# Kernel optimization log

Hardware: AMD Instinct MI355X
Metric: run time of the kernel (lower is better)

The kernel has to match this reference:

```python
import jax, jax.numpy as jnp
import numpy as np

B, C, H, W = 8, 1, 384, 384
P, D, NH, L, E, HF = 16, 768, 12, 12, 4, 3072
Hp, Wp = H // P, W // P
N = Hp * Wp            # 576 tokens
DH = D // NH           # 64 per head
EPS = 1e-5


def setup_inputs() -> dict:
    key = jax.random.key(0)
    ks = jax.random.split(key, 10)
    g = lambda k, shp: (0.02 * jax.random.normal(k, shp, dtype=jnp.float32))
    return {
        "x": jax.random.normal(ks[0], (B, C, H, W), dtype=jnp.float32),
        "patch_w": g(ks[1], (D, C * P * P)),        # Conv2d(k=16,s=16) == unfold+matmul
        "patch_b": jnp.zeros((D,), jnp.float32),
        "pos_embed": g(ks[2], (1, N, D)),
        "ln1_g": jnp.ones((L, D), jnp.float32),
        "ln1_b": jnp.zeros((L, D), jnp.float32),
        "qkv_w": g(ks[3], (L, 3 * D, D)),           # torch MHA in_proj_weight
        "qkv_b": jnp.zeros((L, 3 * D), jnp.float32),
        "out_w": g(ks[4], (L, D, D)),
        "out_b": jnp.zeros((L, D), jnp.float32),
        "ln2_g": jnp.ones((L, D), jnp.float32),
        "ln2_b": jnp.zeros((L, D), jnp.float32),
        "gate_w": g(ks[5], (L, E, D)),
        "gate_b": jnp.zeros((L, E), jnp.float32),
        "w1": g(ks[6], (L, E, HF, D)),
        "b1": jnp.zeros((L, E, HF), jnp.float32),
        "w2": g(ks[7], (L, E, D, HF)),
        "b2": jnp.zeros((L, E, D), jnp.float32),
    }


def _ln(x, g, b):
    m = jnp.mean(x, -1, keepdims=True)
    v = jnp.var(x, -1, keepdims=True)
    return (x - m) * jax.lax.rsqrt(v + EPS) * g + b


def _layer(t, prm):
    (l1g, l1b, qw, qb, ow, ob, l2g, l2b, gw, gb, W1, B1, W2, B2) = prm
    # --- MHA (pre-LN, residual) ---
    h = _ln(t, l1g, l1b)
    qkv = h @ qw.T + qb                                   # [B,N,3D]
    q, k, v = jnp.split(qkv, 3, axis=-1)
    q = q.reshape(B, N, NH, DH).transpose(0, 2, 1, 3)     # [B,NH,N,DH]
    k = k.reshape(B, N, NH, DH).transpose(0, 2, 1, 3)
    v = v.reshape(B, N, NH, DH).transpose(0, 2, 1, 3)
    att = jax.nn.softmax(jnp.einsum('bhnd,bhmd->bhnm', q, k) / jnp.sqrt(jnp.float32(DH)), axis=-1)
    a = jnp.einsum('bhnm,bhmd->bhnd', att, v).transpose(0, 2, 1, 3).reshape(B, N, D)
    t = t + a @ ow.T + ob
    # --- MoE FFN, top_k=1: raw gate logits used as combine weights ---
    h2 = _ln(t, l2g, l2b)
    scores = h2 @ gw.T + gb                               # [B,N,E]
    idx = jnp.argmax(scores, axis=-1)                     # [B,N] chosen expert
    wgt = jnp.max(scores, axis=-1)                        # [B,N] raw logit weight
    hid = jax.nn.gelu(jnp.einsum('bnd,ehd->benh', h2, W1) + B1[None, :, None, :], approximate=False)
    y = jnp.einsum('benh,edh->bend', hid, W2) + B2[None, :, None, :]   # [B,E,N,D]
    sel = jax.nn.one_hot(idx, E, dtype=t.dtype) * wgt[..., None]       # [B,N,E]
    t = t + jnp.einsum('bend,bne->bnd', y, sel)
    return t, None


def reference(x, patch_w, patch_b, pos_embed, ln1_g, ln1_b, qkv_w, qkv_b,
              out_w, out_b, ln2_g, ln2_b, gate_w, gate_b, w1, b1, w2, b2):
    # patch embed: Conv2d(kernel=stride=P) == non-overlapping unfold + matmul
    patches = x.reshape(B, C, Hp, P, Wp, P).transpose(0, 2, 4, 1, 3, 5).reshape(B, N, C * P * P)
    tok = patches @ patch_w.T + patch_b + pos_embed
    layer = jax.checkpoint(_layer)
    tok, _ = jax.lax.scan(layer, tok,
                          (ln1_g, ln1_b, qkv_w, qkv_b, out_w, out_b,
                           ln2_g, ln2_b, gate_w, gate_b, w1, b1, w2, b2))
    # rearrange 'b (h w) c -> b c h w'
    return tok.reshape(B, Hp, Wp, D).transpose(0, 3, 1, 2)
```

## Files before the change

kernel.cpp:

```cpp
#include <hip/hip_runtime.h>
#include <cmath>

#define TOK 4608
#define DMODEL 768

typedef __attribute__((ext_vector_type(8))) _Float16 f16x8;
typedef __attribute__((ext_vector_type(4))) float f32x4;

__device__ __forceinline__ float gelu_exact(float x) {
    return 0.5f * x * (1.0f + erff(x * 0.70710678118654752440f));
}

__device__ __forceinline__ void cvt2(float x, unsigned short& h, unsigned short& m)
{
    _Float16 hf = (_Float16)x;
    float r = (x - (float)hf) * 2048.0f;
    _Float16 mf = (_Float16)r;
    h = __builtin_bit_cast(unsigned short, hf);
    m = __builtin_bit_cast(unsigned short, mf);
}

__device__ __forceinline__ void cvt2_pack8(const float4 a, const float4 b,
                                           uint4& H, uint4& M)
{
    unsigned short h[8], m[8];
    cvt2(a.x, h[0], m[0]); cvt2(a.y, h[1], m[1]);
    cvt2(a.z, h[2], m[2]); cvt2(a.w, h[3], m[3]);
    cvt2(b.x, h[4], m[4]); cvt2(b.y, h[5], m[5]);
    cvt2(b.z, h[6], m[6]); cvt2(b.w, h[7], m[7]);
    H = (uint4){ (unsigned)h[0] | ((unsigned)h[1] << 16), (unsigned)h[2] | ((unsigned)h[3] << 16),
                 (unsigned)h[4] | ((unsigned)h[5] << 16), (unsigned)h[6] | ((unsigned)h[7] << 16) };
    M = (uint4){ (unsigned)m[0] | ((unsigned)m[1] << 16), (unsigned)m[2] | ((unsigned)m[3] << 16),
                 (unsigned)m[4] | ((unsigned)m[5] << 16), (unsigned)m[6] | ((unsigned)m[7] << 16) };
}

__global__ __launch_bounds__(256)
void im2col_kernel(const float* __restrict__ x, float* __restrict__ patches)
{
    int idx = blockIdx.x*256 + threadIdx.x;
    int k = idx & 255, tokid = idx >> 8;
    int b = tokid / 576, n = tokid % 576;
    int hp = n / 24, wp = n % 24;
    patches[idx] = x[(size_t)b*147456 + (size_t)(hp*16 + (k >> 4))*384 + wp*16 + (k & 15)];
}

__global__ __launch_bounds__(256)
void ln_kernel(const float* __restrict__ in, float* __restrict__ out,
               const float* __restrict__ g, const float* __restrict__ bta)
{
    int tokid = blockIdx.x;
    const float* xr = in + (size_t)tokid*768;
    int t = threadIdx.x;
    float v0 = xr[t], v1 = xr[t+256], v2 = xr[t+512];
    float s = v0+v1+v2, q = v0*v0+v1*v1+v2*v2;
    for (int off = 32; off > 0; off >>= 1) {
        s += __shfl_down(s, off);
        q += __shfl_down(q, off);
    }
    __shared__ float ss[4], sq[4];
    int wv = t >> 6, ln = t & 63;
    if (ln == 0) { ss[wv] = s; sq[wv] = q; }
    __syncthreads();
    float ts = ss[0]+ss[1]+ss[2]+ss[3];
    float tq = sq[0]+sq[1]+sq[2]+sq[3];
    float mean = ts * (1.f/768.f);
    float var  = tq * (1.f/768.f) - mean*mean;
    float inv  = rsqrtf(var + 1e-5f);
    float* orow = out + (size_t)tokid*768;
    orow[t]     = (v0-mean)*inv*g[t]     + bta[t];
    orow[t+256] = (v1-mean)*inv*g[t+256] + bta[t+256];
    orow[t+512] = (v2-mean)*inv*g[t+512] + bta[t+512];
}

template<bool SWZ>
__global__ __launch_bounds__(256, 2)
void gemm_big(const float* __restrict__ A, const float* __restrict__ Bw,
              const float* __restrict__ bias, float* __restrict__ C,
              int M, int Nout, int K, int ldA, int ldC, int mode,
              const int* __restrict__ lists, const int* __restrict__ counts,
              const float* __restrict__ wgt)
{
    int Meff = M;
    const int* gather = nullptr;
    if (counts) {
        int e = blockIdx.z;
        Meff   = counts[e];
        gather = lists + e * TOK;
        Bw    += (size_t)e * Nout * K;
        bias  += (size_t)e * Nout;
    }
    int m0, n0;
    if constexpr (SWZ) {
        int gx  = gridDim.x;
        int nwg = gx * gridDim.y;
        int bid = blockIdx.y * gx + blockIdx.x;
        bid = (bid & 7) * (nwg >> 3) + (bid >> 3);
        m0 = (bid / gx) << 7; n0 = (bid % gx) << 7;
    } else {
        m0 = blockIdx.y << 7; n0 = blockIdx.x << 7;
    }
    if (m0 >= Meff) return;

    __shared__ unsigned short Ah[128][40];
    __shared__ unsigned short Am[128][40];
    __shared__ unsigned short Bh[128][40];
    __shared__ unsigned short Bm[128][40];

    int t = threadIdx.x;
    int srow = t >> 1;
    int koff = (t & 1) << 4;

    int ar = m0 + srow;
    long agrow = -1;
    if (ar < Meff) agrow = gather ? gather[ar] : ar;
    const float* Asrc = (agrow >= 0) ? (A + (size_t)agrow*ldA + koff) : nullptr;
    const float* Bsrc = Bw + (size_t)(n0 + srow)*K + koff;

    int lane = t & 63;
    int wv   = t >> 6;
    int wm   = (wv >> 1) << 6;
    int wn   = (wv & 1) << 6;
    int r16  = lane & 15;
    int g    = lane >> 4;

    f32x4 acc1[4][4], acc2[4][4];
    #pragma unroll
    for (int i = 0; i < 4; ++i)
        #pragma unroll
        for (int j = 0; j < 4; ++j) {
            acc1[i][j] = (f32x4){0.f, 0.f, 0.f, 0.f};
            acc2[i][j] = (f32x4){0.f, 0.f, 0.f, 0.f};
        }

    float4 ra[4], rb[4];
    ra[0] = ra[1] = ra[2] = ra[3] = make_float4(0.f, 0.f, 0.f, 0.f);

    auto load_tile = [&](int k0) {
        if (Asrc) {
            ra[0] = *(const float4*)(Asrc + k0);
            ra[1] = *(const float4*)(Asrc + k0 + 4);
            ra[2] = *(const float4*)(Asrc + k0 + 8);
            ra[3] = *(const float4*)(Asrc + k0 + 12);
        }
        rb[0] = *(const float4*)(Bsrc + k0);
        rb[1] = *(const float4*)(Bsrc + k0 + 4);
        rb[2] = *(const float4*)(Bsrc + k0 + 8);
        rb[3] = *(const float4*)(Bsrc + k0 + 12);
    };

    load_tile(0);

    for (int k0 = 0; k0 < K; k0 += 32) {
        __syncthreads();
        {
            uint4 H, M_;
            cvt2_pack8(ra[0], ra[1], H, M_);
            *(uint4*)&Ah[srow][koff]   = H;
            *(uint4*)&Am[srow][koff]   = M_;
            cvt2_pack8(ra[2], ra[3], H, M_);
            *(uint4*)&Ah[srow][koff+8] = H;
            *(uint4*)&Am[srow][koff+8] = M_;
            cvt2_pack8(rb[0], rb[1], H, M_);
            *(uint4*)&Bh[srow][koff]   = H;
            *(uint4*)&Bm[srow][koff]   = M_;
            cvt2_pack8(rb[2], rb[3], H, M_);
            *(uint4*)&Bh[srow][koff+8] = H;
            *(uint4*)&Bm[srow][koff+8] = M_;
        }
        __syncthreads();
        if (k0 + 32 < K) load_tile(k0 + 32);

        f16x8 fah[4], fam[4];
        #pragma unroll
        for (int i = 0; i < 4; ++i) {
            int ml = wm + i*16 + r16;
            fah[i] = *(const f16x8*)&Ah[ml][g*8];
            fam[i] = *(const f16x8*)&Am[ml][g*8];
        }
        #pragma unroll
        for (int j = 0; j < 4; ++j) {
            int nl = wn + j*16 + r16;
            f16x8 fbh = *(const f16x8*)&Bh[nl][g*8];
            f16x8 fbm = *(const f16x8*)&Bm[nl][g*8];
            #pragma unroll
            for (int i = 0; i < 4; ++i) {
                acc1[i][j] = __builtin_amdgcn_mfma_f32_16x16x32_f16(fah[i], fbh, acc1[i][j], 0, 0, 0);
                acc2[i][j] = __builtin_amdgcn_mfma_f32_16x16x32_f16(fah[i], fbm, acc2[i][j], 0, 0, 0);
                acc2[i][j] = __builtin_amdgcn_mfma_f32_16x16x32_f16(fam[i], fbh, acc2[i][j], 0, 0, 0);
            }
        }
    }

    const float MS = 1.0f / 2048.0f;
    float biasv[4];
    #pragma unroll
    for (int j = 0; j < 4; ++j) biasv[j] = bias[n0 + wn + j*16 + r16];

    #pragma unroll
    for (int i = 0; i < 4; ++i) {
        int mb = m0 + wm + i*16 + (g << 2);
        #pragma unroll
        for (int r = 0; r < 4; ++r) {
            int m = mb + r;
            if (m >= Meff) continue;
            int row = gather ? gather[m] : m;
            size_t rowoff = (size_t)row*ldC + n0 + wn + r16;
            float w = (mode == 3) ? wgt[row] : 0.f;
            #pragma unroll
            for (int j = 0; j < 4; ++j) {
                float val = acc1[i][j][r] + acc2[i][j][r] * MS + biasv[j];
                size_t off = rowoff + j*16;
                if      (mode == 0) C[off] = val;
                else if (mode == 1) C[off] += val;
                else if (mode == 2) C[off] = gelu_exact(val);
                else if (mode == 3) C[off] += w * val;
                else C[off] = val + wgt[(size_t)(row % 576)*768 + n0 + wn + j*16 + r16];
            }
        }
    }
}

template<bool SWZ>
__global__ __launch_bounds__(256, 2)
void gemm_small(const float* __restrict__ A, const float* __restrict__ Bw,
                const float* __restrict__ bias, float* __restrict__ C,
                int M, int Nout, int K, int ldA, int ldC, int mode,
                const int* __restrict__ lists, const int* __restrict__ counts,
                const float* __restrict__ wgt)
{
    int Meff = M;
    const int* gather = nullptr;
    if (counts) {
        int e = blockIdx.z;
        Meff   = counts[e];
        gather = lists + e * TOK;
        Bw    += (size_t)e * Nout * K;
        bias  += (size_t)e * Nout;
    }
    int m0, n0;
    if constexpr (SWZ) {
        int gx  = gridDim.x;
        int nwg = gx * gridDim.y;
        int bid = blockIdx.y * gx + blockIdx.x;
        bid = (bid & 7) * (nwg >> 3) + (bid >> 3);
        m0 = (bid / gx) << 6; n0 = (bid % gx) << 6;
    } else {
        m0 = blockIdx.y << 6; n0 = blockIdx.x << 6;
    }
    if (m0 >= Meff) return;

    __shared__ unsigned short Ah[64][72];
    __shared__ unsigned short Am[64][72];
    __shared__ unsigned short Bh[64][72];
    __shared__ unsigned short Bm[64][72];

    int t = threadIdx.x;
    int srow  = t >> 1;
    int khalf = (t & 1) << 5;
    bool isA = srow < 64;
    int row  = isA ? srow : (srow - 64);

    const float* src = nullptr;
    if (isA) {
        int ar = m0 + row;
        if (ar < Meff) {
            long agrow = gather ? gather[ar] : ar;
            src = A + (size_t)agrow*ldA + khalf;
        }
    } else {
        src = Bw + (size_t)(n0 + row)*K + khalf;
    }

    int lane = t & 63;
    int wv   = t >> 6;
    int wm   = (wv >> 1) << 5;
    int wn   = (wv & 1) << 5;
    int r16  = lane & 15;
    int g    = lane >> 4;

    f32x4 acc1[2][2], acc2[2][2];
    #pragma unroll
    for (int i = 0; i < 2; ++i)
        #pragma unroll
        for (int j = 0; j < 2; ++j) {
            acc1[i][j] = (f32x4){0.f, 0.f, 0.f, 0.f};
            acc2[i][j] = (f32x4){0.f, 0.f, 0.f, 0.f};
        }

    float4 rr[8];
    #pragma unroll
    for (int i = 0; i < 8; ++i) rr[i] = make_float4(0.f, 0.f, 0.f, 0.f);

    auto load_tile = [&](int k0) {
        if (src) {
            #pragma unroll
            for (int i = 0; i < 8; ++i) rr[i] = *(const float4*)(src + k0 + 4*i);
        }
    };

    load_tile(0);

    for (int k0 = 0; k0 < K; k0 += 64) {
        __syncthreads();
        {
            unsigned short (*Xh)[72] = isA ? Ah : Bh;
            unsigned short (*Xm)[72] = isA ? Am : Bm;
            #pragma unroll
            for (int i = 0; i < 8; i += 2) {
                uint4 H, M_;
                cvt2_pack8(rr[i], rr[i+1], H, M_);
                *(uint4*)&Xh[row][khalf + 4*i] = H;
                *(uint4*)&Xm[row][khalf + 4*i] = M_;
            }
        }
        __syncthreads();
        if (k0 + 64 < K) load_tile(k0 + 64);

        #pragma unroll
        for (int ks = 0; ks < 2; ++ks) {
            f16x8 fah[2], fam[2];
            #pragma unroll
            for (int i = 0; i < 2; ++i) {
                int ml = wm + i*16 + r16;
                fah[i] = *(const f16x8*)&Ah[ml][ks*32 + g*8];
                fam[i] = *(const f16x8*)&Am[ml][ks*32 + g*8];
            }
            #pragma unroll
            for (int j = 0; j < 2; ++j) {
                int nl = wn + j*16 + r16;
                f16x8 fbh = *(const f16x8*)&Bh[nl][ks*32 + g*8];
                f16x8 fbm = *(const f16x8*)&Bm[nl][ks*32 + g*8];
                #pragma unroll
                for (int i = 0; i < 2; ++i) {
                    acc1[i][j] = __builtin_amdgcn_mfma_f32_16x16x32_f16(fah[i], fbh, acc1[i][j], 0, 0, 0);
                    acc2[i][j] = __builtin_amdgcn_mfma_f32_16x16x32_f16(fah[i], fbm, acc2[i][j], 0, 0, 0);
                    acc2[i][j] = __builtin_amdgcn_mfma_f32_16x16x32_f16(fam[i], fbh, acc2[i][j], 0, 0, 0);
                }
            }
        }
    }

    const float MS = 1.0f / 2048.0f;
    float biasv[2];
    #pragma unroll
    for (int j = 0; j < 2; ++j) biasv[j] = bias[n0 + wn + j*16 + r16];

    #pragma unroll
    for (int i = 0; i < 2; ++i) {
        int mb = m0 + wm + i*16 + (g << 2);
        #pragma unroll
        for (int r = 0; r < 4; ++r) {
            int m = mb + r;
            if (m >= Meff) continue;
            int rowc = gather ? gather[m] : m;
            size_t rowoff = (size_t)rowc*ldC + n0 + wn + r16;
            float w = (mode == 3) ? wgt[rowc] : 0.f;
            #pragma unroll
            for (int j = 0; j < 2; ++j) {
                float val = acc1[i][j][r] + acc2[i][j][r] * MS + biasv[j];
                size_t off = rowoff + j*16;
                if      (mode == 0) C[off] = val;
                else if (mode == 1) C[off] += val;
                else if (mode == 2) C[off] = gelu_exact(val);
                else if (mode == 3) C[off] += w * val;
                else C[off] = val + wgt[(size_t)(rowc % 576)*768 + n0 + wn + j*16 + r16];
            }
        }
    }
}

__global__ __launch_bounds__(256)
void attn_kernel(const float* __restrict__ qkv, float* __restrict__ attn)
{
    int q0 = blockIdx.x << 6;
    int h  = blockIdx.y;
    int b  = blockIdx.z;
    const float* base = qkv + (size_t)b * 576 * 2304;
    int qoff = h << 6, koff = 768 + (h << 6), voff = 1536 + (h << 6);

    __shared__ unsigned short Qh[64][72], Qm[64][72];
    __shared__ unsigned short Kh[64][72], Km[64][72];
    __shared__ unsigned short Vth[64][72], Vtm[64][72];
    __shared__ unsigned short Ph[64][72], Pm[64][72];

    int t    = threadIdx.x;
    int lane = t & 63;
    int wq   = t >> 6;
    int l15  = lane & 15;
    int g    = lane >> 4;

    int srow = t >> 2;
    int sq   = t & 3;

    {
        const float* src = &base[(size_t)(q0 + srow)*2304 + qoff + (sq << 4)];
        #pragma unroll
        for (int k = 0; k < 16; k += 4) {
            float4 v = *(const float4*)(src + k);
            ushort4 hh, mm;
            cvt2(v.x, hh.x, mm.x); cvt2(v.y, hh.y, mm.y);
            cvt2(v.z, hh.z, mm.z); cvt2(v.w, hh.w, mm.w);
            *(ushort4*)&Qh[srow][(sq << 4) + k] = hh;
            *(ushort4*)&Qm[srow][(sq << 4) + k] = mm;
        }
    }
    __syncthreads();

    f16x8 fqh[2], fqm[2];
    #pragma unroll
    for (int ks = 0; ks < 2; ++ks) {
        fqh[ks] = *(const f16x8*)&Qh[wq*16 + l15][ks*32 + g*8];
        fqm[ks] = *(const f16x8*)&Qm[wq*16 + l15][ks*32 + g*8];
    }

    float4 rk[4], rv[4];
    {
        const float* ks_ = &base[(size_t)srow*2304 + koff + (sq << 4)];
        const float* vs_ = &base[(size_t)srow*2304 + voff + (sq << 2)];
        #pragma unroll
        for (int k = 0; k < 4; ++k) rk[k] = *(const float4*)(ks_ + 4*k);
        #pragma unroll
        for (int k = 0; k < 4; ++k) rv[k] = *(const float4*)(vs_ + 16*k);
    }

    f32x4 o1[4], o2[4];
    #pragma unroll
    for (int df = 0; df < 4; ++df) {
        o1[df] = (f32x4){0.f,0.f,0.f,0.f};
        o2[df] = (f32x4){0.f,0.f,0.f,0.f};
    }
    float m_[4] = {-3.4e38f,-3.4e38f,-3.4e38f,-3.4e38f};
    float l_[4] = {0.f,0.f,0.f,0.f};
    const float MS = 1.0f / 2048.0f;

    for (int j0 = 0; j0 < 576; j0 += 64) {
        __syncthreads();
        #pragma unroll
        for (int k = 0; k < 4; ++k) {
            ushort4 hh, mm;
            cvt2(rk[k].x, hh.x, mm.x); cvt2(rk[k].y, hh.y, mm.y);
            cvt2(rk[k].z, hh.z, mm.z); cvt2(rk[k].w, hh.w, mm.w);
            *(ushort4*)&Kh[srow][(sq << 4) + 4*k] = hh;
            *(ushort4*)&Km[srow][(sq << 4) + 4*k] = mm;
        }
        #pragma unroll
        for (int k = 0; k < 4; ++k) {
            ushort4 hh, mm;
            cvt2(rv[k].x, hh.x, mm.x); cvt2(rv[k].y, hh.y, mm.y);
            cvt2(rv[k].z, hh.z, mm.z); cvt2(rv[k].w, hh.w, mm.w);
            int dbase = (sq << 2) + (k << 4);
            Vth[dbase+0][srow] = hh.x; Vtm[dbase+0][srow] = mm.x;
            Vth[dbase+1][srow] = hh.y; Vtm[dbase+1][srow] = mm.y;
            Vth[dbase+2][srow] = hh.z; Vtm[dbase+2][srow] = mm.z;
            Vth[dbase+3][srow] = hh.w; Vtm[dbase+3][srow] = mm.w;
        }
        __syncthreads();
        int jn = j0 + 64;
        if (jn < 576) {
            const float* ks_ = &base[(size_t)(jn + srow)*2304 + koff + (sq << 4)];
            const float* vs_ = &base[(size_t)(jn + srow)*2304 + voff + (sq << 2)];
            #pragma unroll
            for (int k = 0; k < 4; ++k) rk[k] = *(const float4*)(ks_ + 4*k);
            #pragma unroll
            for (int k = 0; k < 4; ++k) rv[k] = *(const float4*)(vs_ + 16*k);
        }

        f32x4 s1[4], s2[4];
        #pragma unroll
        for (int jf = 0; jf < 4; ++jf) {
            s1[jf] = (f32x4){0.f,0.f,0.f,0.f};
            s2[jf] = (f32x4){0.f,0.f,0.f,0.f};
        }
        #pragma unroll
        for (int jf = 0; jf < 4; ++jf) {
            #pragma unroll
            for (int ks = 0; ks < 2; ++ks) {
                f16x8 fkh = *(const f16x8*)&Kh[jf*16 + l15][ks*32 + g*8];
                f16x8 fkm = *(const f16x8*)&Km[jf*16 + l15][ks*32 + g*8];
                s1[jf] = __builtin_amdgcn_mfma_f32_16x16x32_f16(fqh[ks], fkh, s1[jf], 0, 0, 0);
                s2[jf] = __builtin_amdgcn_mfma_f32_16x16x32_f16(fqh[ks], fkm, s2[jf], 0, 0, 0);
                s2[jf] = __builtin_amdgcn_mfma_f32_16x16x32_f16(fqm[ks], fkh, s2[jf], 0, 0, 0);
            }
        }
        float p[4][4];
        #pragma unroll
        for (int jf = 0; jf < 4; ++jf)
            #pragma unroll
            for (int r = 0; r < 4; ++r)
                p[jf][r] = (s1[jf][r] + s2[jf][r]*MS) * 0.125f;

        #pragma unroll
        for (int r = 0; r < 4; ++r) {
            float tm = fmaxf(fmaxf(p[0][r], p[1][r]), fmaxf(p[2][r], p[3][r]));
            #pragma unroll
            for (int off = 8; off > 0; off >>= 1) tm = fmaxf(tm, __shfl_xor(tm, off, 16));
            float mn = fmaxf(m_[r], tm);
            float f  = expf(m_[r] - mn);
            m_[r] = mn;
            l_[r] *= f;
            #pragma unroll
            for (int df = 0; df < 4; ++df) { o1[df][r] *= f; o2[df][r] *= f; }
            float ps = 0.f;
            #pragma unroll
            for (int jf = 0; jf < 4; ++jf) {
                p[jf][r] = expf(p[jf][r] - mn);
                ps += p[jf][r];
            }
            #pragma unroll
            for (int off = 8; off > 0; off >>= 1) ps += __shfl_xor(ps, off, 16);
            l_[r] += ps;
        }
        #pragma unroll
        for (int jf = 0; jf < 4; ++jf)
            #pragma unroll
            for (int r = 0; r < 4; ++r) {
                unsigned short ph, pm;
                cvt2(p[jf][r], ph, pm);
                Ph[wq*16 + g*4 + r][jf*16 + l15] = ph;
                Pm[wq*16 + g*4 + r][jf*16 + l15] = pm;
            }

        #pragma unroll
        for (int ks = 0; ks < 2; ++ks) {
            f16x8 fph = *(const f16x8*)&Ph[wq*16 + l15][ks*32 + g*8];
            f16x8 fpm = *(const f16x8*)&Pm[wq*16 + l15][ks*32 + g*8];
            #pragma unroll
            for (int df = 0; df < 4; ++df) {
                f16x8 fvh = *(const f16x8*)&Vth[df*16 + l15][ks*32 + g*8];
                f16x8 fvm = *(const f16x8*)&Vtm[df*16 + l15][ks*32 + g*8];
                o1[df] = __builtin_amdgcn_mfma_f32_16x16x32_f16(fph, fvh, o1[df], 0, 0, 0);
                o2[df] = __builtin_amdgcn_mfma_f32_16x16x32_f16(fph, fvm, o2[df], 0, 0, 0);
                o2[df] = __builtin_amdgcn_mfma_f32_16x16x32_f16(fpm, fvh, o2[df], 0, 0, 0);
            }
        }
    }

    #pragma unroll
    for (int r = 0; r < 4; ++r) {
        float inv = 1.f / l_[r];
        size_t row = (size_t)(b*576 + q0 + wq*16 + g*4 + r)*768 + qoff + l15;
        #pragma unroll
        for (int df = 0; df < 4; ++df)
            attn[row + df*16] = (o1[df][r] + o2[df][r]*MS) * inv;
    }
}

__global__ __launch_bounds__(256)
void gate_kernel(const float* __restrict__ h2, const float* __restrict__ gw,
                 const float* __restrict__ gb, float* __restrict__ wgt,
                 int* __restrict__ lists, int* __restrict__ counts)
{
    int tokid = blockIdx.x;
    int t = threadIdx.x;
    const float* hr = h2 + (size_t)tokid*768;
    float p0=0.f,p1=0.f,p2=0.f,p3=0.f;
    for (int k = t; k < 768; k += 256) {
        float hv = hr[k];
        p0 = fmaf(hv, gw[k],        p0);
        p1 = fmaf(hv, gw[768 + k],  p1);
        p2 = fmaf(hv, gw[1536 + k], p2);
        p3 = fmaf(hv, gw[2304 + k], p3);
    }
    for (int off = 32; off > 0; off >>= 1) {
        p0 += __shfl_down(p0, off);
        p1 += __shfl_down(p1, off);
        p2 += __shfl_down(p2, off);
        p3 += __shfl_down(p3, off);
    }
    __shared__ float red[4][4];
    int wv = t >> 6, ln = t & 63;
    if (ln == 0) { red[wv][0]=p0; red[wv][1]=p1; red[wv][2]=p2; red[wv][3]=p3; }
    __syncthreads();
    if (t == 0) {
        float s[4];
        #pragma unroll
        for (int e = 0; e < 4; ++e)
            s[e] = red[0][e]+red[1][e]+red[2][e]+red[3][e] + gb[e];
        int best = 0; float bv = s[0];
        #pragma unroll
        for (int e = 1; e < 4; ++e) if (s[e] > bv) { bv = s[e]; best = e; }
        wgt[tokid] = bv;
        int pos = atomicAdd(&counts[best], 1);
        lists[best*TOK + pos] = tokid;
    }
}

__global__ void zero_counts(int* counts) { if (threadIdx.x < 4) counts[threadIdx.x] = 0; }

__global__ __launch_bounds__(256)
void out_transpose(const float* __restrict__ tok, float* __restrict__ out)
{
    int idx = blockIdx.x*256 + threadIdx.x;
    int wp = idx % 24;
    int hp = (idx / 24) % 24;
    int d  = (idx / 576) % 768;
    int b  = idx / (576*768);
    out[idx] = tok[(size_t)(b*576 + hp*24 + wp)*768 + d];
}

extern "C" void kernel_launch(void* const* d_in, const int* in_sizes, int n_in,
                              void* d_out, int out_size, void* d_ws, size_t ws_size,
                              hipStream_t stream)
{
    const float* x       = (const float*)d_in[0];
    const float* patch_w = (const float*)d_in[1];
    const float* patch_b = (const float*)d_in[2];
    const float* pos     = (const float*)d_in[3];
    const float* ln1_g   = (const float*)d_in[4];
    const float* ln1_b   = (const float*)d_in[5];
    const float* qkv_w   = (const float*)d_in[6];
    const float* qkv_b   = (const float*)d_in[7];
    const float* out_w   = (const float*)d_in[8];
    const float* out_b   = (const float*)d_in[9];
    const float* ln2_g   = (const float*)d_in[10];
    const float* ln2_b   = (const float*)d_in[11];
    const float* gate_w  = (const float*)d_in[12];
    const float* gate_b  = (const float*)d_in[13];
    const float* w1      = (const float*)d_in[14];
    const float* b1      = (const float*)d_in[15];
    const float* w2      = (const float*)d_in[16];
    const float* b2      = (const float*)d_in[17];
    float* out = (float*)d_out;

    float* ws    = (float*)d_ws;
    float* tok   = ws;
    float* h     = ws + 3538944;
    float* scr   = ws + 7077888;
    float* qkv   = scr;
    float* attn  = scr + 10616832;
    float* hid   = scr;
    float* patches = scr;
    float* wgt   = ws + 21233664;
    int*   lists = (int*)(ws + 21238272);
    int*   counts= (int*)(ws + 21256704);

    im2col_kernel<<<4608, 256, 0, stream>>>(x, patches);
    gemm_small<true><<<dim3(12,72,1), 256, 0, stream>>>(patches, patch_w, patch_b, tok,
                                                        4608, 768, 256, 256, 768, 4,
                                                        nullptr, nullptr, pos);

    for (int l = 0; l < 12; ++l) {
        ln_kernel<<<4608, 256, 0, stream>>>(tok, h, ln1_g + l*768, ln1_b + l*768);
        gemm_big<true><<<dim3(18,36,1), 256, 0, stream>>>(h, qkv_w + (size_t)l*1769472,
                                                          qkv_b + l*2304, qkv,
                                                          4608, 2304, 768, 768, 2304, 0,
                                                          nullptr, nullptr, nullptr);
        attn_kernel<<<dim3(9,12,8), 256, 0, stream>>>(qkv, attn);
        gemm_small<true><<<dim3(12,72,1), 256, 0, stream>>>(attn, out_w + (size_t)l*589824,
                                                            out_b + l*768, tok,
                                                            4608, 768, 768, 768, 768, 1,
                                                            nullptr, nullptr, nullptr);
        ln_kernel<<<4608, 256, 0, stream>>>(tok, h, ln2_g + l*768, ln2_b + l*768);
        zero_counts<<<1, 64, 0, stream>>>(counts);
        gate_kernel<<<4608, 256, 0, stream>>>(h, gate_w + l*3072, gate_b + l*4, wgt, lists, counts);
        gemm_big<false><<<dim3(24,36,4), 256, 0, stream>>>(h, w1 + (size_t)l*9437184,
                                                           b1 + (size_t)l*4*3072, hid,
                                                           4608, 3072, 768, 768, 3072, 2,
                                                           lists, counts, nullptr);
        gemm_small<false><<<dim3(12,72,4), 256, 0, stream>>>(hid, w2 + (size_t)l*9437184,
                                                             b2 + (size_t)l*4*768, tok,
                                                             4608, 768, 3072, 3072, 768, 3,
                                                             lists, counts, wgt);
    }
    out_transpose<<<13824, 256, 0, stream>>>(tok, out);
}
```

Baseline: 8.257 ms.

## Double-buffer shared-memory tiles in split-fp16 GEMM kernels to drop one barrier

Both GEMM kernels now keep two shared-memory buffers per operand. The next tile is converted and stored into the alternate buffer after the MFMA work on the current one, so only one __syncthreads is needed per k-step instead of two. The aim is to cut barrier stalls and overlap staging with compute. In exchange, shared-memory use per block doubles, which may reduce occupancy.

```diff
diff --git a/kernel.cpp b/kernel.cpp
--- a/kernel.cpp
+++ b/kernel.cpp
@@ -101,10 +101,10 @@
     }
     if (m0 >= Meff) return;
 
-    __shared__ unsigned short Ah[128][40];
-    __shared__ unsigned short Am[128][40];
-    __shared__ unsigned short Bh[128][40];
-    __shared__ unsigned short Bm[128][40];
+    __shared__ unsigned short Ah[2][128][40];
+    __shared__ unsigned short Am[2][128][40];
+    __shared__ unsigned short Bh[2][128][40];
+    __shared__ unsigned short Bm[2][128][40];
 
     int t = threadIdx.x;
     int srow = t >> 1;
@@ -148,40 +148,43 @@
         rb[3] = *(const float4*)(Bsrc + k0 + 12);
     };
 
+    auto stage = [&](int buf) {
+        uint4 H, M_;
+        cvt2_pack8(ra[0], ra[1], H, M_);
+        *(uint4*)&Ah[buf][srow][koff]   = H;
+        *(uint4*)&Am[buf][srow][koff]   = M_;
+        cvt2_pack8(ra[2], ra[3], H, M_);
+        *(uint4*)&Ah[buf][srow][koff+8] = H;
+        *(uint4*)&Am[buf][srow][koff+8] = M_;
+        cvt2_pack8(rb[0], rb[1], H, M_);
+        *(uint4*)&Bh[buf][srow][koff]   = H;
+        *(uint4*)&Bm[buf][srow][koff]   = M_;
+        cvt2_pack8(rb[2], rb[3], H, M_);
+        *(uint4*)&Bh[buf][srow][koff+8] = H;
+        *(uint4*)&Bm[buf][srow][koff+8] = M_;
+    };
+
     load_tile(0);
+    stage(0);
+    int cur = 0;
 
     for (int k0 = 0; k0 < K; k0 += 32) {
         __syncthreads();
-        {
-            uint4 H, M_;
-            cvt2_pack8(ra[0], ra[1], H, M_);
-            *(uint4*)&Ah[srow][koff]   = H;
-            *(uint4*)&Am[srow][koff]   = M_;
-            cvt2_pack8(ra[2], ra[3], H, M_);
-            *(uint4*)&Ah[srow][koff+8] = H;
-            *(uint4*)&Am[srow][koff+8] = M_;
-            cvt2_pack8(rb[0], rb[1], H, M_);
-            *(uint4*)&Bh[srow][koff]   = H;
-            *(uint4*)&Bm[srow][koff]   = M_;
-            cvt2_pack8(rb[2], rb[3], H, M_);
-            *(uint4*)&Bh[srow][koff+8] = H;
-            *(uint4*)&Bm[srow][koff+8] = M_;
-        }
-        __syncthreads();
-        if (k0 + 32 < K) load_tile(k0 + 32);
+        bool more = (k0 + 32 < K);
+        if (more) load_tile(k0 + 32);
 
         f16x8 fah[4], fam[4];
         #pragma unroll
         for (int i = 0; i < 4; ++i) {
             int ml = wm + i*16 + r16;
-            fah[i] = *(const f16x8*)&Ah[ml][g*8];
-            fam[i] = *(const f16x8*)&Am[ml][g*8];
+            fah[i] = *(const f16x8*)&Ah[cur][ml][g*8];
+            fam[i] = *(const f16x8*)&Am[cur][ml][g*8];
         }
         #pragma unroll
         for (int j = 0; j < 4; ++j) {
             int nl = wn + j*16 + r16;
-            f16x8 fbh = *(const f16x8*)&Bh[nl][g*8];
-            f16x8 fbm = *(const f16x8*)&Bm[nl][g*8];
+            f16x8 fbh = *(const f16x8*)&Bh[cur][nl][g*8];
+            f16x8 fbm = *(const f16x8*)&Bm[cur][nl][g*8];
             #pragma unroll
             for (int i = 0; i < 4; ++i) {
                 acc1[i][j] = __builtin_amdgcn_mfma_f32_16x16x32_f16(fah[i], fbh, acc1[i][j], 0, 0, 0);
@@ -189,6 +192,8 @@
                 acc2[i][j] = __builtin_amdgcn_mfma_f32_16x16x32_f16(fam[i], fbh, acc2[i][j], 0, 0, 0);
             }
         }
+        if (more) stage(cur ^ 1);
+        cur ^= 1;
     }
 
     const float MS = 1.0f / 2048.0f;
@@ -249,10 +254,10 @@
     }
     if (m0 >= Meff) return;
 
-    __shared__ unsigned short Ah[64][72];
-    __shared__ unsigned short Am[64][72];
-    __shared__ unsigned short Bh[64][72];
-    __shared__ unsigned short Bm[64][72];
+    __shared__ unsigned short Ah[2][64][72];
+    __shared__ unsigned short Am[2][64][72];
+    __shared__ unsigned short Bh[2][64][72];
+    __shared__ unsigned short Bm[2][64][72];
 
     int t = threadIdx.x;
     int srow  = t >> 1;
@@ -298,23 +303,26 @@
         }
     };
 
+    auto stage = [&](int buf) {
+        unsigned short (*Xh)[72] = isA ? Ah[buf] : Bh[buf];
+        unsigned short (*Xm)[72] = isA ? Am[buf] : Bm[buf];
+        #pragma unroll
+        for (int i = 0; i < 8; i += 2) {
+            uint4 H, M_;
+            cvt2_pack8(rr[i], rr[i+1], H, M_);
+            *(uint4*)&Xh[row][khalf + 4*i] = H;
+            *(uint4*)&Xm[row][khalf + 4*i] = M_;
+        }
+    };
+
     load_tile(0);
+    stage(0);
+    int cur = 0;
 
     for (int k0 = 0; k0 < K; k0 += 64) {
         __syncthreads();
-        {
-            unsigned short (*Xh)[72] = isA ? Ah : Bh;
-            unsigned short (*Xm)[72] = isA ? Am : Bm;
-            #pragma unroll
-            for (int i = 0; i < 8; i += 2) {
-                uint4 H, M_;
-                cvt2_pack8(rr[i], rr[i+1], H, M_);
-                *(uint4*)&Xh[row][khalf + 4*i] = H;
-                *(uint4*)&Xm[row][khalf + 4*i] = M_;
-            }
-        }
-        __syncthreads();
-        if (k0 + 64 < K) load_tile(k0 + 64);
+        bool more = (k0 + 64 < K);
+        if (more) load_tile(k0 + 64);
 
         #pragma unroll
         for (int ks = 0; ks < 2; ++ks) {
@@ -322,14 +330,14 @@
             #pragma unroll
             for (int i = 0; i < 2; ++i) {
                 int ml = wm + i*16 + r16;
-                fah[i] = *(const f16x8*)&Ah[ml][ks*32 + g*8];
-                fam[i] = *(const f16x8*)&Am[ml][ks*32 + g*8];
+                fah[i] = *(const f16x8*)&Ah[cur][ml][ks*32 + g*8];
+                fam[i] = *(const f16x8*)&Am[cur][ml][ks*32 + g*8];
             }
             #pragma unroll
             for (int j = 0; j < 2; ++j) {
                 int nl = wn + j*16 + r16;
-                f16x8 fbh = *(const f16x8*)&Bh[nl][ks*32 + g*8];
-                f16x8 fbm = *(const f16x8*)&Bm[nl][ks*32 + g*8];
+                f16x8 fbh = *(const f16x8*)&Bh[cur][nl][ks*32 + g*8];
+                f16x8 fbm = *(const f16x8*)&Bm[cur][nl][ks*32 + g*8];
                 #pragma unroll
                 for (int i = 0; i < 2; ++i) {
                     acc1[i][j] = __builtin_amdgcn_mfma_f32_16x16x32_f16(fah[i], fbh, acc1[i][j], 0, 0, 0);
@@ -338,6 +346,8 @@
                 }
             }
         }
+        if (more) stage(cur ^ 1);
+        cur ^= 1;
     }
 
     const float MS = 1.0f / 2048.0f;
```

Measured after the change: 9.186 ms. +11.2%, slower.
